# Kernel optimization log

Hardware: AMD Instinct MI355X
Metric: run time of the kernel (lower is better)

## Reference

```python
import jax, jax.numpy as jnp
import numpy as np
from jax import lax

B, L, K, OUT = 16384, 8192, 2, 128
L3 = L - 3 * (K - 1)  # 8189, length after 3 valid convs


def setup_inputs() -> dict:
    key = jax.random.key(0)
    ks = jax.random.split(key, 9)
    return {
        "x": jax.random.normal(ks[0], (B, 1, L), jnp.float32),
        "w1": jax.random.normal(ks[1], (1, 1, K), jnp.float32),
        "b1": jax.random.normal(ks[2], (1,), jnp.float32),
        "w2": jax.random.normal(ks[3], (1, 1, K), jnp.float32),
        "b2": jax.random.normal(ks[4], (1,), jnp.float32),
        "w3": jax.random.normal(ks[5], (1, 1, K), jnp.float32),
        "b3": jax.random.normal(ks[6], (1,), jnp.float32),
        "W": jax.random.normal(ks[7], (OUT, L3), jnp.float32) * 0.02,
        "b": jax.random.normal(ks[8], (OUT,), jnp.float32),
    }


def _conv1d(x, w, b):
    # x: [B, 1, L_in], w: [1, 1, K] (OIW), valid padding, stride 1
    y = lax.conv_general_dilated(x, w, window_strides=(1,), padding="VALID",
                                 dimension_numbers=("NCW", "OIW", "NCW"))
    return y + b[None, :, None]


def reference(x, w1, b1, w2, b2, w3, b3, W, b):
    h = jax.nn.relu(_conv1d(x, w1, b1))
    h = jax.nn.relu(_conv1d(h, w2, b2))
    h = jax.nn.relu(_conv1d(h, w3, b3))
    flat = h.reshape(h.shape[0], -1)          # [B, L3]
    return flat @ W.T + b                     # [B, OUT]
```

## Files before the change

### kernel.cpp

```cpp
#include <hip/hip_runtime.h>
#include <hip/hip_bf16.h>

typedef __attribute__((ext_vector_type(8))) short short8;
typedef __attribute__((ext_vector_type(8))) unsigned short ushort8;
typedef __attribute__((ext_vector_type(4))) float f32x4;

#define LIN  8192
#define L3V  8189
#define NOUT 128
#define KP   8192
#define BM   64
#define BK   128
#define NT   (KP / BK)
#define PITCH (BK + 8)

static __device__ __forceinline__ unsigned short f2bf(float f) {
    union { float f; unsigned u; } c; c.f = f;
    unsigned r = c.u + 0x7FFFu + ((c.u >> 16) & 1u);
    return (unsigned short)(r >> 16);
}

__global__ void wprep(const float* __restrict__ W, unsigned short* __restrict__ Wb) {
    int idx = blockIdx.x * 256 + threadIdx.x;
    int n = idx >> 13;
    int k = idx & (KP - 1);
    float v = (k < L3V) ? W[(size_t)n * L3V + k] : 0.0f;
    Wb[idx] = f2bf(v);
}

__global__ __launch_bounds__(512, 2) void fused(
    const float* __restrict__ x,
    const float* __restrict__ w1, const float* __restrict__ b1,
    const float* __restrict__ w2, const float* __restrict__ b2,
    const float* __restrict__ w3, const float* __restrict__ b3,
    const unsigned short* __restrict__ Wb,
    const float* __restrict__ bias,
    float* __restrict__ out)
{
    __shared__ unsigned short hA[2][BM * PITCH];
    __shared__ unsigned short wA[2][NOUT * PITCH];

    const int tid  = threadIdx.x;
    const int row0 = blockIdx.x * BM;

    const float w10 = w1[0], w11 = w1[1], cb1 = b1[0];
    const float w20 = w2[0], w21 = w2[1], cb2 = b2[0];
    const float w30 = w3[0], w31 = w3[1], cb3 = b3[0];

    const int srow = tid >> 3;
    const int scol = (tid & 7) * 16;
    const float* xrow = x + (size_t)(row0 + srow) * LIN;

    const int wn = tid >> 2;
    const int wq = tid & 3;
    const unsigned short* wrow = Wb + (size_t)wn * KP + wq * 32;

    const int lane = tid & 63;
    const int wid  = tid >> 6;
    const int wr   = wid >> 1;
    const int wc   = wid & 1;
    const int l15  = lane & 15;
    const int koff = (lane >> 4) * 8;
    const int arow_off = (wr * 16 + l15) * PITCH + koff;

    f32x4 acc[4];
    #pragma unroll
    for (int f = 0; f < 4; ++f) acc[f] = (f32x4){0.f, 0.f, 0.f, 0.f};

    float   xv[20];
    ushort8 wv[4];

    auto stage_load = [&](int t) {
        const int gk = t * BK + scol;
        if (gk + 20 <= LIN) {
            #pragma unroll
            for (int q = 0; q < 5; ++q) {
                const float4 v = *reinterpret_cast<const float4*>(xrow + gk + q * 4);
                xv[q*4+0] = v.x; xv[q*4+1] = v.y; xv[q*4+2] = v.z; xv[q*4+3] = v.w;
            }
        } else {
            #pragma unroll
            for (int q = 0; q < 4; ++q) {
                const float4 v = *reinterpret_cast<const float4*>(xrow + gk + q * 4);
                xv[q*4+0] = v.x; xv[q*4+1] = v.y; xv[q*4+2] = v.z; xv[q*4+3] = v.w;
            }
            xv[16] = 0.f; xv[17] = 0.f; xv[18] = 0.f; xv[19] = 0.f;
        }
        const ushort8* wsrc = reinterpret_cast<const ushort8*>(wrow + t * BK);
        #pragma unroll
        for (int i = 0; i < 4; ++i) wv[i] = wsrc[i];
    };

    auto stage_store = [&](int t, int s) {
        const int gk = t * BK + scol;
        float h1[18];
        #pragma unroll
        for (int j = 0; j < 18; ++j)
            h1[j] = fmaxf(fmaf(w10, xv[j], fmaf(w11, xv[j+1], cb1)), 0.0f);
        float h2[17];
        #pragma unroll
        for (int j = 0; j < 17; ++j)
            h2[j] = fmaxf(fmaf(w20, h1[j], fmaf(w21, h1[j+1], cb2)), 0.0f);
        ushort8 hp[2];
        #pragma unroll
        for (int j = 0; j < 16; ++j) {
            float h3 = fmaxf(fmaf(w30, h2[j], fmaf(w31, h2[j+1], cb3)), 0.0f);
            unsigned short u = (gk + j < L3V) ? f2bf(h3) : (unsigned short)0;
            hp[j >> 3][j & 7] = u;
        }
        ushort8* hd = reinterpret_cast<ushort8*>(&hA[s][srow * PITCH + scol]);
        hd[0] = hp[0];
        hd[1] = hp[1];
        ushort8* wdst = reinterpret_cast<ushort8*>(&wA[s][wn * PITCH + wq * 32]);
        #pragma unroll
        for (int i = 0; i < 4; ++i) wdst[i] = wv[i];
    };

    stage_load(0);
    stage_store(0, 0);
    stage_load(1);
    __syncthreads();

    int sel = 0;
    for (int t = 0; t < NT; ++t) {
        const unsigned short* hB = hA[sel];
        const unsigned short* wB = wA[sel];
        #pragma unroll
        for (int kk = 0; kk < BK; kk += 32) {
            const short8 af = *reinterpret_cast<const short8*>(&hB[arow_off + kk]);
            #pragma unroll
            for (int f = 0; f < 4; ++f) {
                const int bn = wc * 64 + f * 16 + l15;
                const short8 bf = *reinterpret_cast<const short8*>(&wB[bn * PITCH + kk + koff]);
                acc[f] = __builtin_amdgcn_mfma_f32_16x16x32_bf16(af, bf, acc[f], 0, 0, 0);
            }
        }
        if (t + 1 < NT) stage_store(t + 1, sel ^ 1);
        if (t + 2 < NT) stage_load(t + 2);
        __syncthreads();
        sel ^= 1;
    }

    #pragma unroll
    for (int f = 0; f < 4; ++f) {
        const int col = wc * 64 + f * 16 + l15;
        const float bv = bias[col];
        #pragma unroll
        for (int j = 0; j < 4; ++j) {
            const int grow = row0 + wr * 16 + (lane >> 4) * 4 + j;
            out[(size_t)grow * NOUT + col] = acc[f][j] + bv;
        }
    }
}

extern "C" void kernel_launch(void* const* d_in, const int* in_sizes, int n_in,
                              void* d_out, int out_size, void* d_ws, size_t ws_size,
                              hipStream_t stream) {
    const float* x  = (const float*)d_in[0];
    const float* w1 = (const float*)d_in[1];
    const float* b1 = (const float*)d_in[2];
    const float* w2 = (const float*)d_in[3];
    const float* b2 = (const float*)d_in[4];
    const float* w3 = (const float*)d_in[5];
    const float* b3 = (const float*)d_in[6];
    const float* W  = (const float*)d_in[7];
    const float* b  = (const float*)d_in[8];
    float* out = (float*)d_out;
    unsigned short* Wb = (unsigned short*)d_ws;

    wprep<<<dim3((NOUT * KP) / 256), dim3(256), 0, stream>>>(W, Wb);
    fused<<<dim3(16384 / BM), dim3(512), 0, stream>>>(
        x, w1, b1, w2, b2, w3, b3, Wb, b, out);
}
```

Baseline: 142.9 us.

## Deepen register prefetch to two stages with ping-pong register buffers

Adds a second set of register staging buffers and unrolls the main loop by two, so global loads for tile t+2 are issued before the MFMA work on tile t rather than after it. The longer window lets global memory latency overlap with the matrix math and the LDS stores. The cost is higher register pressure under the 512-thread, 2-blocks-per-CU launch bound, which could cause spills.

```diff
diff --git a/kernel.cpp b/kernel.cpp
--- a/kernel.cpp
+++ b/kernel.cpp
@@ -67,10 +67,10 @@
     #pragma unroll
     for (int f = 0; f < 4; ++f) acc[f] = (f32x4){0.f, 0.f, 0.f, 0.f};
 
-    float   xv[20];
-    ushort8 wv[4];
+    float   xvA[20], xvB[20];
+    ushort8 wvA[4], wvB[4];
 
-    auto stage_load = [&](int t) {
+    auto stage_load = [&](int t, float (&xv)[20], ushort8 (&wv)[4]) {
         const int gk = t * BK + scol;
         if (gk + 20 <= LIN) {
             #pragma unroll
@@ -91,7 +91,7 @@
         for (int i = 0; i < 4; ++i) wv[i] = wsrc[i];
     };
 
-    auto stage_store = [&](int t, int s) {
+    auto stage_store = [&](int t, int s, float (&xv)[20], ushort8 (&wv)[4]) {
         const int gk = t * BK + scol;
         float h1[18];
         #pragma unroll
@@ -116,15 +116,9 @@
         for (int i = 0; i < 4; ++i) wdst[i] = wv[i];
     };
 
-    stage_load(0);
-    stage_store(0, 0);
-    stage_load(1);
-    __syncthreads();
-
-    int sel = 0;
-    for (int t = 0; t < NT; ++t) {
-        const unsigned short* hB = hA[sel];
-        const unsigned short* wB = wA[sel];
+    auto mfma_tile = [&](int s) {
+        const unsigned short* hB = hA[s];
+        const unsigned short* wB = wA[s];
         #pragma unroll
         for (int kk = 0; kk < BK; kk += 32) {
             const short8 af = *reinterpret_cast<const short8*>(&hB[arow_off + kk]);
@@ -135,10 +129,23 @@
                 acc[f] = __builtin_amdgcn_mfma_f32_16x16x32_bf16(af, bf, acc[f], 0, 0, 0);
             }
         }
-        if (t + 1 < NT) stage_store(t + 1, sel ^ 1);
-        if (t + 2 < NT) stage_load(t + 2);
+    };
+
+    stage_load(0, xvA, wvA);
+    stage_store(0, 0, xvA, wvA);
+    stage_load(1, xvA, wvA);
+    __syncthreads();
+
+    #pragma unroll 1
+    for (int t = 0; t < NT; t += 2) {
+        if (t + 2 < NT) stage_load(t + 2, xvB, wvB);
+        mfma_tile(0);
+        if (t + 1 < NT) stage_store(t + 1, 1, xvA, wvA);
         __syncthreads();
-        sel ^= 1;
+        if (t + 3 < NT) stage_load(t + 3, xvA, wvA);
+        mfma_tile(1);
+        if (t + 2 < NT) stage_store(t + 2, 0, xvB, wvB);
+        __syncthreads();
     }
 
     #pragma unroll
```

Result: slower. 178.4 us (+24.8%).
